# Optimization experiments

Measured on AMD Instinct MI355X. Metric: run time of the kernel, lower is better.

Reference implementation:

```python
import jax, jax.numpy as jnp
import numpy as np

R_MAX = 10.0
NUM_BESSEL = 8
POLY_P = 5
EMB = 64
MLP_DIM = 256
NUM_LAYERS = 3
IN_DIM = 10
OUT_DIM = 1
N_NODES = 256
N_EDGES = 1024
N_GRAPHS = 16
# gated TP output: 0e channel carries 64 scalars + 128 gates (one per gated 1o/2e irrep)
GATE_MUL = {0: 3 * EMB, 1: EMB, 2: EMB}
L0_PATHS = [(0, 0, 0), (0, 1, 1), (0, 2, 2)]  # in_irreps = 64x0e
LN_PATHS = [(0, 0, 0), (1, 1, 0), (2, 2, 0), (0, 1, 1), (1, 0, 1), (1, 2, 1), (2, 1, 1), (0, 2, 2), (2, 0, 2), (1, 1, 2), (2, 2, 2)]

def _npaths(paths):
    d = {0: 0, 1: 0, 2: 0}
    for _, _, l3 in paths:
        d[l3] += 1
    return d

L0_NP = _npaths(L0_PATHS)
LN_NP = _npaths(LN_PATHS)
L0_NUMEL = sum(EMB * GATE_MUL[l3] for _, _, l3 in L0_PATHS)   # 20480
LN_NUMEL = sum(EMB * GATE_MUL[l3] for _, _, l3 in LN_PATHS)   # 69632

# ---- real spherical harmonics, component normalization (||Y_l||^2 = 2l+1) ----
def _sh_np(v):
    x, y, z = v[:, 0], v[:, 1], v[:, 2]
    s15 = np.sqrt(15.0)
    return {0: np.ones((v.shape[0], 1)),
            1: np.sqrt(3.0) * np.stack([x, y, z], 1),
            2: np.stack([s15 * x * y, s15 * y * z, 0.5 * np.sqrt(5.0) * (3 * z * z - 1), s15 * x * z, 0.5 * s15 * (x * x - y * y)], 1)}

def _rot(axis, t):
    c, s = np.cos(t), np.sin(t)
    R = np.eye(3)
    i, j = [(1, 2), (2, 0), (0, 1)][axis]
    R[i, i] = c; R[j, j] = c; R[i, j] = -s; R[j, i] = s
    return R

_PTS = np.random.RandomState(0).randn(64, 3)
_PTS /= np.linalg.norm(_PTS, axis=1, keepdims=True)

def _D(l, R):
    # rep matrix D with Y(Rv) = D @ Y(v), fit by least squares over sample points
    A = _sh_np(_PTS)[l]
    B = _sh_np(_PTS @ R.T)[l]
    return np.linalg.lstsq(A, B, rcond=None)[0].T

def _gen(l, axis, eps=1e-4):
    return (_D(l, _rot(axis, eps)) - _D(l, _rot(axis, -eps))) / (2 * eps)

def _cg(l1, l2, l3):
    # Clebsch-Gordan tensor as null space of the infinitesimal equivariance constraint
    d1, d2, d3 = 2 * l1 + 1, 2 * l2 + 1, 2 * l3 + 1
    rows = []
    for a in range(3):
        J1, J2, J3 = _gen(l1, a), _gen(l2, a), _gen(l3, a)
        rows.append(np.kron(J1.T, np.eye(d2 * d3)) + np.kron(np.eye(d1), np.kron(J2.T, np.eye(d3))) - np.kron(np.eye(d1 * d2), J3))
    _, _, Vh = np.linalg.svd(np.vstack(rows))
    c = Vh[-1].reshape(d1, d2, d3)
    c = c / np.linalg.norm(c)
    c = c * np.sign(c.flat[int(np.argmax(np.abs(c)))])
    return c

CG = {p: jnp.asarray(_cg(*p), jnp.float32) for p in set(LN_PATHS)}

def _sh_jax(u):
    x, y, z = u[..., 0], u[..., 1], u[..., 2]
    s15 = 15.0 ** 0.5
    return {0: jnp.ones_like(x)[:, None],
            1: (3.0 ** 0.5) * jnp.stack([x, y, z], -1),
            2: jnp.stack([s15 * x * y, s15 * y * z, 0.5 * (5.0 ** 0.5) * (3 * z * z - 1), s15 * x * z, 0.5 * s15 * (x * x - y * y)], -1)}

def _radial(r):
    # Bessel radial basis * polynomial cutoff envelope (MACE-style RadialEmbeddingBlock)
    n = jnp.arange(1, NUM_BESSEL + 1, dtype=r.dtype)
    bessel = (2.0 / R_MAX) ** 0.5 * jnp.sin(n * jnp.pi * r[:, None] / R_MAX) / r[:, None]
    x = r / R_MAX
    p = POLY_P
    env = 1.0 - 0.5 * (p + 1) * (p + 2) * x ** p + p * (p + 2) * x ** (p + 1) - 0.5 * p * (p + 1) * x ** (p + 2)
    env = env * (x < 1.0)
    return bessel * env[:, None]

def _conv(h, sh, ef, recv, send, paths, n_per, w1, b1, w2, b2):
    # TensorProductConvLayer: MLP(edge_feats) -> TP weights, CG tensor product, scatter-sum, gate
    E = ef.shape[0]
    w = jax.nn.relu(ef @ w1 + b1) @ w2 + b2  # (E, weight_numel)
    msgs = {0: 0.0, 1: 0.0, 2: 0.0}
    off = 0
    for (l1, l2, l3) in paths:
        mv = GATE_MUL[l3]
        wp = w[:, off:off + EMB * mv].reshape(E, EMB, mv)
        off += EMB * mv
        tmp = jnp.einsum('eui,ej,ijk->euk', h[l1][send], sh[l2], CG[(l1, l2, l3)])
        alpha = float(1.0 / np.sqrt(EMB * n_per[l3]))  # fan-in path normalization
        msgs[l3] = msgs[l3] + alpha * jnp.einsum('euk,euv->evk', tmp, wp)
    agg = {l: jax.ops.segment_sum(msgs[l], recv, num_segments=N_NODES) for l in msgs}
    s = agg[0][..., 0]  # (N, 192): 64 scalars + 128 gates
    return {0: jax.nn.silu(s[:, :EMB])[:, :, None],
            1: agg[1] * jax.nn.sigmoid(s[:, EMB:2 * EMB])[:, :, None],
            2: agg[2] * jax.nn.sigmoid(s[:, 2 * EMB:])[:, :, None]}

def _forward(atoms, pos, edge_index, batch, emb, l0_fc1_w, l0_fc1_b, l0_fc2_w, l0_fc2_b, fcs1_w, fcs1_b, fcs2_w, fcs2_b, pred_w1, pred_b1, pred_w2, pred_b2):
    recv, send = edge_index[0], edge_index[1]
    vec = pos[recv] - pos[send]
    r = jnp.maximum(jnp.linalg.norm(vec, axis=-1), 1e-6)
    sh = _sh_jax(vec / r[:, None])
    ef = _radial(r)
    h = {0: emb[atoms][:, :, None]}  # (N, 64, 1) scalar features
    h_new = _conv(h, sh, ef, recv, send, L0_PATHS, L0_NP, l0_fc1_w, l0_fc1_b, l0_fc2_w, l0_fc2_b)
    h_new[0] = h_new[0] + h[0]  # residual; F.pad means only scalar block overlaps
    h = h_new
    for i in range(NUM_LAYERS - 1):
        h_new = _conv(h, sh, ef, recv, send, LN_PATHS, LN_NP, fcs1_w[i], fcs1_b[i], fcs2_w[i], fcs2_b[i])
        h = {l: h_new[l] + h[l] for l in h_new}
    pooled = jax.ops.segment_sum(h[0][..., 0], batch, num_segments=N_GRAPHS)  # out[:, :emb_dim]
    return jax.nn.relu(pooled @ pred_w1 + pred_b1) @ pred_w2 + pred_b2

def setup_inputs():
    key = jax.random.key(0)
    ks = jax.random.split(key, 12)
    def lin(k, fi, fo):
        return jax.random.normal(k, (fi, fo), jnp.float32) * float(1.0 / np.sqrt(fi))
    return dict(
        atoms=jax.random.randint(ks[0], (N_NODES,), 0, IN_DIM),
        pos=jax.random.normal(ks[1], (N_NODES, 3), jnp.float32) * 2.0,
        edge_index=jax.random.randint(ks[2], (2, N_EDGES), 0, N_NODES),
        batch=jnp.sort(jax.random.randint(ks[3], (N_NODES,), 0, N_GRAPHS)),
        emb=jax.random.normal(ks[4], (IN_DIM, EMB), jnp.float32),
        l0_fc1_w=lin(ks[5], NUM_BESSEL, MLP_DIM), l0_fc1_b=jnp.zeros((MLP_DIM,), jnp.float32),
        l0_fc2_w=lin(ks[6], MLP_DIM, L0_NUMEL), l0_fc2_b=jnp.zeros((L0_NUMEL,), jnp.float32),
        fcs1_w=jax.random.normal(ks[7], (NUM_LAYERS - 1, NUM_BESSEL, MLP_DIM), jnp.float32) * float(1.0 / np.sqrt(NUM_BESSEL)),
        fcs1_b=jnp.zeros((NUM_LAYERS - 1, MLP_DIM), jnp.float32),
        fcs2_w=jax.random.normal(ks[8], (NUM_LAYERS - 1, MLP_DIM, LN_NUMEL), jnp.float32) * float(1.0 / np.sqrt(MLP_DIM)),
        fcs2_b=jnp.zeros((NUM_LAYERS - 1, LN_NUMEL), jnp.float32),
        pred_w1=lin(ks[9], EMB, EMB), pred_b1=jnp.zeros((EMB,), jnp.float32),
        pred_w2=lin(ks[10], EMB, OUT_DIM), pred_b2=jnp.zeros((OUT_DIM,), jnp.float32),
    )

def reference(atoms, pos, edge_index, batch, emb, l0_fc1_w, l0_fc1_b, l0_fc2_w, l0_fc2_b, fcs1_w, fcs1_b, fcs2_w, fcs2_b, pred_w1, pred_b1, pred_w2, pred_b2):
    return _forward(atoms, pos, edge_index, batch, emb, l0_fc1_w, l0_fc1_b, l0_fc2_w, l0_fc2_b, fcs1_w, fcs1_b, fcs2_w, fcs2_b, pred_w1, pred_b1, pred_w2, pred_b2)
```

## Files before the change

### kernel.cpp

```cpp
#include <hip/hip_runtime.h>
#include <hip/hip_bf16.h>
#include <math.h>

#define NE 1024
#define NN 256
#define NG 16
#define EMB 64
#define KD 256
#define BK 64
#define NUMEL_L0 20480
#define NUMEL_LN 69632
#define MSGW 704
#define MAXE 256

typedef __attribute__((ext_vector_type(8))) __bf16 bf16x8;
typedef __attribute__((ext_vector_type(4))) float f32x4;
typedef __attribute__((ext_vector_type(4))) unsigned int u32x4;

__device__ __align__(16) float g_sh[NE * 8];
__device__ __align__(16) float g_ef[NE * 8];
__device__ __align__(16) unsigned short g_hidb[3][NE * KD];
__device__ __align__(16) unsigned short g_w2t0[(size_t)NUMEL_L0 * KD];
__device__ __align__(16) unsigned short g_w2t1[(size_t)NUMEL_LN * KD];
__device__ __align__(16) unsigned short g_w2t2[(size_t)NUMEL_LN * KD];
__device__ __align__(16) unsigned short g_wb0[(size_t)NE * NUMEL_L0];
__device__ __align__(16) unsigned short g_wb1[(size_t)NE * NUMEL_LN];
__device__ __align__(16) unsigned short g_wb2[(size_t)NE * NUMEL_LN];
__device__ __align__(16) float g_msgs[NE * MSGW];
__device__ __align__(16) float g_h0[NN * EMB];
__device__ __align__(16) float g_h1[NN * EMB * 3];
__device__ __align__(16) float g_h2[NN * EMB * 5];
__device__ int g_elist[NN * MAXE];
__device__ int g_ecnt[NN];
__device__ float g_cg[363];

__device__ __forceinline__ unsigned short f2b(float x) {
    __hip_bfloat16 h = __float2bfloat16(x);
    return *(unsigned short*)&h;
}
__device__ __forceinline__ float b2f(unsigned short u) {
    __hip_bfloat16 h;
    *(unsigned short*)&h = u;
    return __bfloat162float(h);
}

__device__ __forceinline__ void gld16(const void* g, void* l) {
    __builtin_amdgcn_global_load_lds(
        (const __attribute__((address_space(1))) unsigned int*)g,
        (__attribute__((address_space(3))) unsigned int*)l, 16, 0, 0);
}

struct Path { int l1, l2, d1, d2, d3, mv, off, cgoff, tmpoff; };

__constant__ Path PLN[11] = {
    {0, 0, 1, 1, 1, 192, 0,     0,   0},
    {1, 1, 3, 3, 1, 192, 12288, 1,   64},
    {2, 2, 5, 5, 1, 192, 24576, 10,  128},
    {0, 1, 1, 3, 3, 64,  36864, 35,  192},
    {1, 0, 3, 1, 3, 64,  40960, 44,  384},
    {1, 2, 3, 5, 3, 64,  45056, 53,  576},
    {2, 1, 5, 3, 3, 64,  49152, 98,  768},
    {0, 2, 1, 5, 5, 64,  53248, 143, 960},
    {2, 0, 5, 1, 5, 64,  57344, 168, 1280},
    {1, 1, 3, 3, 5, 64,  61440, 193, 1600},
    {2, 2, 5, 5, 5, 64,  65536, 238, 1920},
};
__constant__ Path PL0[3] = {
    {0, 0, 1, 1, 1, 192, 0,     0,   0},
    {0, 1, 1, 3, 3, 64,  12288, 35,  64},
    {0, 2, 1, 5, 5, 64,  16384, 143, 256},
};

__device__ void init_cg_body() {
    for (int i = 0; i < 363; i++) g_cg[i] = 0.f;
    const float K3 = 0.57735026918962576f;
    const float K5 = 0.44721359549995794f;
    const float A  = 0.31622776601683794f;
    const float B  = 0.18257418583505536f;
    const float C2 = 0.36514837167011072f;
    const float P  = 0.23904572186687872f;
    const float Q  = 0.20701966780270626f;
    const float S  = 0.11952286093343936f;
    g_cg[0] = 1.f;
    for (int i = 0; i < 3; i++) g_cg[1 + i * 3 + i] = K3;
    for (int i = 0; i < 5; i++) g_cg[10 + i * 5 + i] = K5;
    for (int i = 0; i < 3; i++) g_cg[35 + i * 3 + i] = K3;
    for (int i = 0; i < 3; i++) g_cg[44 + i * 3 + i] = K3;
    g_cg[53 + 1]  = A;  g_cg[53 + 15] = A;  g_cg[53 + 20] = A;
    g_cg[53 + 34] = A;  g_cg[53 + 11] = A;  g_cg[53 + 39] = A;
    g_cg[53 + 6]  = -B; g_cg[53 + 22] = -B; g_cg[53 + 38] = C2;
    g_cg[53 + 12] = A;  g_cg[53 + 28] = -A;
    g_cg[98 + 1]  = A;  g_cg[98 + 3]  = A;  g_cg[98 + 14] = A;
    g_cg[98 + 16] = A;  g_cg[98 + 29] = A;  g_cg[98 + 33] = A;
    g_cg[98 + 18] = -B; g_cg[98 + 22] = -B; g_cg[98 + 26] = C2;
    g_cg[98 + 36] = A;  g_cg[98 + 40] = -A;
    for (int i = 0; i < 5; i++) g_cg[143 + i * 5 + i] = K5;
    for (int i = 0; i < 5; i++) g_cg[168 + i * 5 + i] = K5;
    g_cg[193 + 5]  = A;  g_cg[193 + 15] = A;  g_cg[193 + 26] = A;
    g_cg[193 + 36] = A;  g_cg[193 + 13] = A;  g_cg[193 + 33] = A;
    g_cg[193 + 2]  = -B; g_cg[193 + 22] = -B; g_cg[193 + 42] = C2;
    g_cg[193 + 4]  = A;  g_cg[193 + 24] = -A;
    g_cg[238 + 2]   = P;  g_cg[238 + 10]  = P;  g_cg[238 + 50]  = P;
    g_cg[238 + 8]   = -Q; g_cg[238 + 16]  = -Q; g_cg[238 + 28]  = -Q;
    g_cg[238 + 40]  = -Q; g_cg[238 + 76]  = -Q; g_cg[238 + 80]  = -Q;
    g_cg[238 + 32]  = -S; g_cg[238 + 36]  = -S; g_cg[238 + 56]  = -S;
    g_cg[238 + 34]  = Q;  g_cg[238 + 46]  = Q;  g_cg[238 + 106] = Q;
    g_cg[238 + 62]  = -P;
    g_cg[238 + 74]  = P;  g_cg[238 + 114] = P;  g_cg[238 + 122] = P;
    g_cg[238 + 68]  = -S; g_cg[238 + 88]  = -S; g_cg[238 + 92]  = -S;
    g_cg[238 + 94]  = -Q; g_cg[238 + 98]  = -Q; g_cg[238 + 118] = -Q;
}

__global__ __launch_bounds__(256) void k_setup(const int* ei, const float* pos,
                                               const int* atoms, const float* emb) {
    int bid = blockIdx.x, tid = threadIdx.x;
    if (bid == 0) {
        if (tid == 0) init_cg_body();
        return;
    }
    if (bid <= 4) {
        int e = (bid - 1) * 256 + tid;
        int recv = ei[e], send = ei[NE + e];
        float vx = pos[recv * 3 + 0] - pos[send * 3 + 0];
        float vy = pos[recv * 3 + 1] - pos[send * 3 + 1];
        float vz = pos[recv * 3 + 2] - pos[send * 3 + 2];
        float rn = sqrtf(vx * vx + vy * vy + vz * vz);
        float r = fmaxf(rn, 1e-6f);
        float x = vx / r, y = vy / r, z = vz / r;
        const float S3 = 1.7320508075688772f;
        const float S15 = 3.8729833462074170f;
        const float S5H = 1.1180339887498949f;
        const float S15H = 1.9364916731037085f;
        g_sh[e * 8 + 0] = S3 * x;
        g_sh[e * 8 + 1] = S3 * y;
        g_sh[e * 8 + 2] = S3 * z;
        g_sh[e * 8 + 3] = S15 * x * y;
        g_sh[e * 8 + 4] = S15 * y * z;
        g_sh[e * 8 + 5] = S5H * (3.f * z * z - 1.f);
        g_sh[e * 8 + 6] = S15 * x * z;
        g_sh[e * 8 + 7] = S15H * (x * x - y * y);
        float xr = r * 0.1f;
        float env = 0.f;
        if (xr < 1.f) {
            float x5 = xr * xr * xr * xr * xr;
            env = 1.f - 21.f * x5 + 35.f * x5 * xr - 15.f * x5 * xr * xr;
        }
        const float SB = 0.44721359549995794f;
        const float PI = 3.14159265358979323846f;
        for (int nb = 1; nb <= 8; nb++) {
            g_ef[e * 8 + nb - 1] = SB * sinf((float)nb * PI * r * 0.1f) / r * env;
        }
        return;
    }
    if (bid <= 68) {
        int idx = (bid - 5) * 256 + tid;
        int n = idx / EMB, u = idx % EMB;
        g_h0[idx] = emb[atoms[n] * EMB + u];
        for (int k = 0; k < 3; k++) g_h1[idx * 3 + k] = 0.f;
        for (int k = 0; k < 5; k++) g_h2[idx * 5 + k] = 0.f;
        return;
    }
    {
        int n = bid - 69;
        int lane = tid & 63, w = tid >> 6;
        __shared__ int wsum[4];
        int mask = 0;
#pragma unroll
        for (int i = 0; i < 4; i++) {
            if (ei[tid * 4 + i] == n) mask |= 1 << i;
        }
        int nm = __popc(mask);
        int incl = nm;
#pragma unroll
        for (int off = 1; off < 64; off <<= 1) {
            int v = __shfl_up(incl, off);
            if (lane >= off) incl += v;
        }
        if (lane == 63) wsum[w] = incl;
        __syncthreads();
        int wbase = 0;
        for (int i = 0; i < w; i++) wbase += wsum[i];
        int base = wbase + incl - nm;
#pragma unroll
        for (int i = 0; i < 4; i++) {
            if (mask & (1 << i)) g_elist[n * MAXE + base++] = tid * 4 + i;
        }
        if (tid == 255) g_ecnt[n] = wbase + incl;
    }
}

__global__ __launch_bounds__(256) void k_w2t_hid_all(
        const float* l0w2, const float* f2w,
        const float* l0w1, const float* l0b1, const float* f1w, const float* f1b) {
    __shared__ float t[32][33];
    int bid = blockIdx.x;
    if (bid < 39936) {
        int layer, lbid, numel;
        const float* w2;
        unsigned short* dst;
        if (bid < 5120)       { layer = 0; lbid = bid;          numel = NUMEL_L0; w2 = l0w2; dst = g_w2t0; }
        else if (bid < 22528) { layer = 1; lbid = bid - 5120;   numel = NUMEL_LN; w2 = f2w;  dst = g_w2t1; }
        else                  { layer = 2; lbid = bid - 22528;  numel = NUMEL_LN;
                                w2 = f2w + (size_t)KD * NUMEL_LN; dst = g_w2t2; }
        int n0 = (lbid >> 3) * 32, k0 = (lbid & 7) * 32;
        int tx = threadIdx.x & 31, ty = threadIdx.x >> 5;
#pragma unroll
        for (int i = 0; i < 4; i++) {
            int kl = ty * 4 + i;
            t[kl][tx] = w2[(size_t)(k0 + kl) * numel + n0 + tx];
        }
        __syncthreads();
#pragma unroll
        for (int i = 0; i < 4; i++) {
            int nl = ty * 4 + i;
            dst[(size_t)(n0 + nl) * KD + k0 + tx] = f2b(t[tx][nl]);
        }
    } else {
        int r = bid - 39936;
        int layer = r >> 10, e = r & 1023;
        const float* w1 = layer == 0 ? l0w1 : f1w + (size_t)(layer - 1) * 8 * KD;
        const float* b1 = layer == 0 ? l0b1 : f1b + (size_t)(layer - 1) * KD;
        int m = threadIdx.x;
        float acc = b1[m];
        for (int nb = 0; nb < 8; nb++) acc += g_ef[e * 8 + nb] * w1[nb * KD + m];
        g_hidb[layer][e * KD + m] = f2b(fmaxf(acc, 0.f));
    }
}

__global__ __launch_bounds__(256) void k_gemm_all(const float* l0b2, const float* f2b_) {
    __shared__ unsigned short S[16384];
    int tid = threadIdx.x;
    int lane = tid & 63, wid = tid >> 6;
    int wm = wid >> 1, wn = wid & 1;
    int id = blockIdx.x;
    int layer, lid, numel;
    const unsigned short* hidb;
    const unsigned short* w2t;
    unsigned short* wb;
    const float* b2;
    if (id < 4352)      { layer = 2; lid = id;        numel = NUMEL_LN; hidb = g_hidb[2]; w2t = g_w2t2; wb = g_wb2; b2 = f2b_ + NUMEL_LN; }
    else if (id < 8704) { layer = 1; lid = id - 4352; numel = NUMEL_LN; hidb = g_hidb[1]; w2t = g_w2t1; wb = g_wb1; b2 = f2b_; }
    else                { layer = 0; lid = id - 8704; numel = NUMEL_L0; hidb = g_hidb[0]; w2t = g_w2t0; wb = g_wb0; b2 = l0b2; }
    int xcd = lid & 7;
    int q = lid >> 3;
    int mb = q & 7;
    int ytile = q >> 3;
    int nt = xcd + 8 * ytile;
    int m0 = mb * 128, n0 = nt * 128;
    int fr = lane & 15;
    int ko = (lane >> 4) * 8;

    const char* gA = (const char*)hidb;
    const char* gB = (const char*)w2t;
    f32x4 acc[4][4] = {};

    for (int kst = 0; kst < 4; kst++) {
#pragma unroll
        for (int i = 0; i < 4; i++) {
            int L = wid * 4096 + i * 1024 + lane * 16;
            int row = L >> 7, p = L & 127;
            int sp = p ^ ((row & 7) << 4);
            gld16(gA + ((size_t)(m0 + row) * KD + kst * BK) * 2 + sp, (char*)S + L);
        }
#pragma unroll
        for (int i = 0; i < 4; i++) {
            int L = wid * 4096 + i * 1024 + lane * 16;
            int row = L >> 7, p = L & 127;
            int sp = p ^ ((row & 7) << 4);
            gld16(gB + ((size_t)(n0 + row) * KD + kst * BK) * 2 + sp, (char*)S + 16384 + L);
        }
        __syncthreads();
#pragma unroll
        for (int ks = 0; ks < 2; ks++) {
            int klb = ks * 64 + ko * 2;
            bf16x8 af[4], bf_[4];
#pragma unroll
            for (int f = 0; f < 4; f++) {
                int ra = wm * 64 + f * 16 + fr;
                af[f] = *(bf16x8*)((char*)S + ra * 128 + (klb ^ ((ra & 7) << 4)));
                int rb = wn * 64 + f * 16 + fr;
                bf_[f] = *(bf16x8*)((char*)S + 16384 + rb * 128 + (klb ^ ((rb & 7) << 4)));
            }
#pragma unroll
            for (int i = 0; i < 4; i++)
#pragma unroll
                for (int j = 0; j < 4; j++)
                    acc[i][j] = __builtin_amdgcn_mfma_f32_16x16x32_bf16(af[i], bf_[j], acc[i][j], 0, 0, 0);
        }
        __syncthreads();
    }

#pragma unroll
    for (int j = 0; j < 4; j++) {
        int colL = wn * 64 + j * 16 + fr;
        float bb = b2[n0 + colL];
#pragma unroll
        for (int i = 0; i < 4; i++) {
#pragma unroll
            for (int r = 0; r < 4; r++) {
                int rowL = wm * 64 + i * 16 + (lane >> 4) * 4 + r;
                *(unsigned short*)((char*)S + rowL * 256 + ((colL * 2) ^ ((rowL & 7) << 4))) =
                    f2b(acc[i][j][r] + bb);
            }
        }
    }
    __syncthreads();
    for (int c = tid; c < 2048; c += 256) {
        int row = c >> 4, p16 = (c & 15) * 16;
        u32x4 v = *(u32x4*)((char*)S + row * 256 + (p16 ^ ((row & 7) << 4)));
        *(u32x4*)((char*)(wb + (size_t)(m0 + row) * numel + n0) + p16) = v;
    }
}

__global__ __launch_bounds__(256) void k_contract(const int* ei, int layer) {
    int e = blockIdx.x;
    int grp = blockIdx.y;
    int tid = threadIdx.x;
    __shared__ float tmp[1280];
    int layer0 = (layer == 0) ? 1 : 0;
    int numel = layer0 ? NUMEL_L0 : NUMEL_LN;
    const unsigned short* wbase = layer == 0 ? g_wb0 : (layer == 1 ? g_wb1 : g_wb2);
    const Path* PT = layer0 ? PL0 : PLN;
    int npaths = layer0 ? 3 : 11;
    int pstart = layer0 ? grp : (grp == 0 ? 0 : (grp == 1 ? 3 : 7));
    int pend   = layer0 ? grp + 1 : (grp == 0 ? 3 : (grp == 1 ? 7 : 11));
    int tbase = PT[pstart].tmpoff;
    int tend  = (pend < npaths) ? PT[pend].tmpoff : (layer0 ? 576 : 2240);
    int ttot = tend - tbase;
    const unsigned short* wrow = wbase + (size_t)e * numel;
    int send = ei[NE + e];

    for (int t = tid; t < ttot; t += 256) {
        int tt = t + tbase;
        int p = pend - 1;
        while (tt < PT[p].tmpoff) p--;
        Path pp = PT[p];
        int rem = tt - pp.tmpoff;
        int u = rem / pp.d3, k = rem % pp.d3;
        float acc = 0.f;
        for (int i = 0; i < pp.d1; i++) {
            float hv = (pp.l1 == 0) ? g_h0[send * EMB + u]
                     : (pp.l1 == 1) ? g_h1[(send * EMB + u) * 3 + i]
                                    : g_h2[(send * EMB + u) * 5 + i];
            for (int j = 0; j < pp.d2; j++) {
                float sv = (pp.l2 == 0) ? 1.f
                         : (pp.l2 == 1 ? g_sh[e * 8 + j] : g_sh[e * 8 + 3 + j]);
                acc += hv * sv * g_cg[pp.cgoff + (i * pp.d2 + j) * pp.d3 + k];
            }
        }
        tmp[t] = acc;
    }
    __syncthreads();

    float alpha0 = layer0 ? 0.125f : 0.07216878364870323f;
    float alpha12 = layer0 ? 0.125f : 0.0625f;
    int v3 = tid / 3, k3 = tid - v3 * 3;
    int v5a = tid / 5, k5a = tid - v5a * 5;
    int p5b = 256 + tid;
    int v5b = p5b / 5, k5b = p5b - v5b * 5;
    float a0 = 0.f, a1 = 0.f;

    for (int p = pstart; p < pend; p++) {
        Path pp = PT[p];
        int to = pp.tmpoff - tbase;
        const unsigned short* wp = wrow + pp.off;
        if (pp.d3 == 1) {
            if (tid < 192) {
#pragma unroll 16
                for (int u = 0; u < 64; u++)
                    a0 += tmp[to + u] * b2f(wp[u * 192 + tid]);
            }
        } else if (pp.d3 == 3) {
            if (tid < 192) {
#pragma unroll 16
                for (int u = 0; u < 64; u++)
                    a0 += tmp[to + u * 3 + k3] * b2f(wp[u * 64 + v3]);
            }
        } else {
#pragma unroll 16
            for (int u = 0; u < 64; u++)
                a0 += tmp[to + u * 5 + k5a] * b2f(wp[u * 64 + v5a]);
            if (tid < 64) {
#pragma unroll 16
                for (int u = 0; u < 64; u++)
                    a1 += tmp[to + u * 5 + k5b] * b2f(wp[u * 64 + v5b]);
            }
        }
    }
    if (grp == 0) {
        if (tid < 192) g_msgs[e * MSGW + tid] = alpha0 * a0;
    } else if (grp == 1) {
        if (tid < 192) g_msgs[e * MSGW + 192 + tid] = alpha12 * a0;
    } else {
        g_msgs[e * MSGW + 384 + tid] = alpha12 * a0;
        if (tid < 64) g_msgs[e * MSGW + 640 + tid] = alpha12 * a1;
    }
}

__global__ __launch_bounds__(256) void k_agggate() {
    int n = blockIdx.x, tid = threadIdx.x;
    __shared__ float agg[MSGW];
    int cnt = g_ecnt[n];
    for (int d = tid; d < MSGW; d += 256) {
        float a = 0.f;
        for (int idx = 0; idx < cnt; idx++) {
            int e = g_elist[n * MAXE + idx];
            a += g_msgs[e * MSGW + d];
        }
        agg[d] = a;
    }
    __syncthreads();
    if (tid < EMB) {
        int u = tid;
        float s0 = agg[u], s1 = agg[64 + u], s2 = agg[128 + u];
        float sg0 = 1.f / (1.f + expf(-s0));
        float g0 = s0 * sg0;
        float sg1 = 1.f / (1.f + expf(-s1));
        float sg2 = 1.f / (1.f + expf(-s2));
        g_h0[n * EMB + u] += g0;
        for (int k = 0; k < 3; k++) g_h1[(n * EMB + u) * 3 + k] += agg[192 + u * 3 + k] * sg1;
        for (int k = 0; k < 5; k++) g_h2[(n * EMB + u) * 5 + k] += agg[384 + u * 5 + k] * sg2;
    }
}

__global__ __launch_bounds__(1024) void k_poolhead(const int* batch, const float* w1,
                                                   const float* b1, const float* w2,
                                                   const float* b2, float* out) {
    __shared__ float pl[NG * EMB];
    int g = threadIdx.x >> 6, u = threadIdx.x & 63;
    float a = 0.f;
    for (int n = 0; n < NN; n++)
        if (batch[n] == g) a += g_h0[n * EMB + u];
    pl[g * EMB + u] = a;
    __syncthreads();
    float t = b1[u];
    for (int uu = 0; uu < EMB; uu++) t += pl[g * EMB + uu] * w1[uu * EMB + u];
    t = fmaxf(t, 0.f);
    float contrib = t * w2[u];
    for (int off = 32; off > 0; off >>= 1) contrib += __shfl_down(contrib, off);
    if (u == 0) out[g] = contrib + b2[0];
}

extern "C" void kernel_launch(void* const* d_in, const int* in_sizes, int n_in,
                              void* d_out, int out_size, void* d_ws, size_t ws_size,
                              hipStream_t stream) {
    const int* atoms = (const int*)d_in[0];
    const float* pos = (const float*)d_in[1];
    const int* ei = (const int*)d_in[2];
    const int* batch = (const int*)d_in[3];
    const float* emb = (const float*)d_in[4];
    const float* l0w1 = (const float*)d_in[5];
    const float* l0b1 = (const float*)d_in[6];
    const float* l0w2 = (const float*)d_in[7];
    const float* l0b2 = (const float*)d_in[8];
    const float* f1w = (const float*)d_in[9];
    const float* f1b = (const float*)d_in[10];
    const float* f2w = (const float*)d_in[11];
    const float* f2b_ = (const float*)d_in[12];
    const float* pw1 = (const float*)d_in[13];
    const float* pb1 = (const float*)d_in[14];
    const float* pw2 = (const float*)d_in[15];
    const float* pb2 = (const float*)d_in[16];
    float* out = (float*)d_out;

    k_setup<<<dim3(325), dim3(256), 0, stream>>>(ei, pos, atoms, emb);
    k_w2t_hid_all<<<dim3(43008), dim3(256), 0, stream>>>(l0w2, f2w, l0w1, l0b1, f1w, f1b);
    k_gemm_all<<<dim3(9984), dim3(256), 0, stream>>>(l0b2, f2b_);

    for (int layer = 0; layer < 3; layer++) {
        k_contract<<<dim3(NE, 3), dim3(256), 0, stream>>>(ei, layer);
        k_agggate<<<dim3(NN), dim3(256), 0, stream>>>();
    }

    k_poolhead<<<dim3(1), dim3(1024), 0, stream>>>(batch, pw1, pb1, pw2, pb2, out);
}
```

Before: 474.5 us.

## Run per-layer weight GEMM just before contraction with a shared output buffer

Replaces the single batched GEMM that produced all three layers' per-edge weight tensors with one GEMM launch per layer, issued right before that layer's contraction. All three layers now write into one shared bf16 buffer, so a freshly written weight tensor is likely still in cache when the contraction reads it, and the global footprint shrinks. The weight transpose is merged into the setup kernel and the hidden-layer MLP gets its own kernel. In exchange there are more launches, and the per-layer GEMMs are serialized with the contraction and aggregation kernels instead of running as one large grid.

```diff
diff --git a/kernel.cpp b/kernel.cpp
--- a/kernel.cpp
+++ b/kernel.cpp
@@ -23,9 +23,7 @@
 __device__ __align__(16) unsigned short g_w2t0[(size_t)NUMEL_L0 * KD];
 __device__ __align__(16) unsigned short g_w2t1[(size_t)NUMEL_LN * KD];
 __device__ __align__(16) unsigned short g_w2t2[(size_t)NUMEL_LN * KD];
-__device__ __align__(16) unsigned short g_wb0[(size_t)NE * NUMEL_L0];
-__device__ __align__(16) unsigned short g_wb1[(size_t)NE * NUMEL_LN];
-__device__ __align__(16) unsigned short g_wb2[(size_t)NE * NUMEL_LN];
+__device__ __align__(16) unsigned short g_wb[(size_t)NE * NUMEL_LN];
 __device__ __align__(16) float g_msgs[NE * MSGW];
 __device__ __align__(16) float g_h0[NN * EMB];
 __device__ __align__(16) float g_h1[NN * EMB * 3];
@@ -112,7 +110,8 @@
 }
 
 __global__ __launch_bounds__(256) void k_setup(const int* ei, const float* pos,
-                                               const int* atoms, const float* emb) {
+                                               const int* atoms, const float* emb,
+                                               const float* l0w2, const float* f2w) {
     int bid = blockIdx.x, tid = threadIdx.x;
     if (bid == 0) {
         if (tid == 0) init_cg_body();
@@ -160,7 +159,7 @@
         for (int k = 0; k < 5; k++) g_h2[idx * 5 + k] = 0.f;
         return;
     }
-    {
+    if (bid <= 324) {
         int n = bid - 69;
         int lane = tid & 63, w = tid >> 6;
         __shared__ int wsum[4];
@@ -186,24 +185,20 @@
             if (mask & (1 << i)) g_elist[n * MAXE + base++] = tid * 4 + i;
         }
         if (tid == 255) g_ecnt[n] = wbase + incl;
-    }
-}
-
-__global__ __launch_bounds__(256) void k_w2t_hid_all(
-        const float* l0w2, const float* f2w,
-        const float* l0w1, const float* l0b1, const float* f1w, const float* f1b) {
-    __shared__ float t[32][33];
-    int bid = blockIdx.x;
-    if (bid < 39936) {
-        int layer, lbid, numel;
+        return;
+    }
+    {
+        __shared__ float t[32][33];
+        int wbid = bid - 325;
+        int lbid, numel;
         const float* w2;
         unsigned short* dst;
-        if (bid < 5120)       { layer = 0; lbid = bid;          numel = NUMEL_L0; w2 = l0w2; dst = g_w2t0; }
-        else if (bid < 22528) { layer = 1; lbid = bid - 5120;   numel = NUMEL_LN; w2 = f2w;  dst = g_w2t1; }
-        else                  { layer = 2; lbid = bid - 22528;  numel = NUMEL_LN;
-                                w2 = f2w + (size_t)KD * NUMEL_LN; dst = g_w2t2; }
+        if (wbid < 5120)       { lbid = wbid;         numel = NUMEL_L0; w2 = l0w2; dst = g_w2t0; }
+        else if (wbid < 22528) { lbid = wbid - 5120;  numel = NUMEL_LN; w2 = f2w;  dst = g_w2t1; }
+        else                   { lbid = wbid - 22528; numel = NUMEL_LN;
+                                 w2 = f2w + (size_t)KD * NUMEL_LN; dst = g_w2t2; }
         int n0 = (lbid >> 3) * 32, k0 = (lbid & 7) * 32;
-        int tx = threadIdx.x & 31, ty = threadIdx.x >> 5;
+        int tx = tid & 31, ty = tid >> 5;
 #pragma unroll
         for (int i = 0; i < 4; i++) {
             int kl = ty * 4 + i;
@@ -215,34 +210,29 @@
             int nl = ty * 4 + i;
             dst[(size_t)(n0 + nl) * KD + k0 + tx] = f2b(t[tx][nl]);
         }
-    } else {
-        int r = bid - 39936;
-        int layer = r >> 10, e = r & 1023;
-        const float* w1 = layer == 0 ? l0w1 : f1w + (size_t)(layer - 1) * 8 * KD;
-        const float* b1 = layer == 0 ? l0b1 : f1b + (size_t)(layer - 1) * KD;
-        int m = threadIdx.x;
-        float acc = b1[m];
-        for (int nb = 0; nb < 8; nb++) acc += g_ef[e * 8 + nb] * w1[nb * KD + m];
-        g_hidb[layer][e * KD + m] = f2b(fmaxf(acc, 0.f));
-    }
-}
-
-__global__ __launch_bounds__(256) void k_gemm_all(const float* l0b2, const float* f2b_) {
+    }
+}
+
+__global__ __launch_bounds__(256) void k_hid_all(const float* l0w1, const float* l0b1,
+                                                 const float* f1w, const float* f1b) {
+    int r = blockIdx.x;
+    int layer = r >> 10, e = r & 1023;
+    const float* w1 = layer == 0 ? l0w1 : f1w + (size_t)(layer - 1) * 8 * KD;
+    const float* b1 = layer == 0 ? l0b1 : f1b + (size_t)(layer - 1) * KD;
+    int m = threadIdx.x;
+    float acc = b1[m];
+    for (int nb = 0; nb < 8; nb++) acc += g_ef[e * 8 + nb] * w1[nb * KD + m];
+    g_hidb[layer][e * KD + m] = f2b(fmaxf(acc, 0.f));
+}
+
+__global__ __launch_bounds__(256) void k_gemm_mfma(const float* b2, int numel, int layer) {
     __shared__ unsigned short S[16384];
     int tid = threadIdx.x;
     int lane = tid & 63, wid = tid >> 6;
     int wm = wid >> 1, wn = wid & 1;
     int id = blockIdx.x;
-    int layer, lid, numel;
-    const unsigned short* hidb;
-    const unsigned short* w2t;
-    unsigned short* wb;
-    const float* b2;
-    if (id < 4352)      { layer = 2; lid = id;        numel = NUMEL_LN; hidb = g_hidb[2]; w2t = g_w2t2; wb = g_wb2; b2 = f2b_ + NUMEL_LN; }
-    else if (id < 8704) { layer = 1; lid = id - 4352; numel = NUMEL_LN; hidb = g_hidb[1]; w2t = g_w2t1; wb = g_wb1; b2 = f2b_; }
-    else                { layer = 0; lid = id - 8704; numel = NUMEL_L0; hidb = g_hidb[0]; w2t = g_w2t0; wb = g_wb0; b2 = l0b2; }
-    int xcd = lid & 7;
-    int q = lid >> 3;
+    int xcd = id & 7;
+    int q = id >> 3;
     int mb = q & 7;
     int ytile = q >> 3;
     int nt = xcd + 8 * ytile;
@@ -250,7 +240,8 @@
     int fr = lane & 15;
     int ko = (lane >> 4) * 8;
 
-    const char* gA = (const char*)hidb;
+    const unsigned short* w2t = layer == 0 ? g_w2t0 : (layer == 1 ? g_w2t1 : g_w2t2);
+    const char* gA = (const char*)g_hidb[layer];
     const char* gB = (const char*)w2t;
     f32x4 acc[4][4] = {};
 
@@ -308,7 +299,7 @@
     for (int c = tid; c < 2048; c += 256) {
         int row = c >> 4, p16 = (c & 15) * 16;
         u32x4 v = *(u32x4*)((char*)S + row * 256 + (p16 ^ ((row & 7) << 4)));
-        *(u32x4*)((char*)(wb + (size_t)(m0 + row) * numel + n0) + p16) = v;
+        *(u32x4*)((char*)(g_wb + (size_t)(m0 + row) * numel + n0) + p16) = v;
     }
 }
 
@@ -319,7 +310,6 @@
     __shared__ float tmp[1280];
     int layer0 = (layer == 0) ? 1 : 0;
     int numel = layer0 ? NUMEL_L0 : NUMEL_LN;
-    const unsigned short* wbase = layer == 0 ? g_wb0 : (layer == 1 ? g_wb1 : g_wb2);
     const Path* PT = layer0 ? PL0 : PLN;
     int npaths = layer0 ? 3 : 11;
     int pstart = layer0 ? grp : (grp == 0 ? 0 : (grp == 1 ? 3 : 7));
@@ -327,7 +317,7 @@
     int tbase = PT[pstart].tmpoff;
     int tend  = (pend < npaths) ? PT[pend].tmpoff : (layer0 ? 576 : 2240);
     int ttot = tend - tbase;
-    const unsigned short* wrow = wbase + (size_t)e * numel;
+    const unsigned short* wrow = g_wb + (size_t)e * numel;
     int send = ei[NE + e];
 
     for (int t = tid; t < ttot; t += 256) {
@@ -463,11 +453,13 @@
     const float* pb2 = (const float*)d_in[16];
     float* out = (float*)d_out;
 
-    k_setup<<<dim3(325), dim3(256), 0, stream>>>(ei, pos, atoms, emb);
-    k_w2t_hid_all<<<dim3(43008), dim3(256), 0, stream>>>(l0w2, f2w, l0w1, l0b1, f1w, f1b);
-    k_gemm_all<<<dim3(9984), dim3(256), 0, stream>>>(l0b2, f2b_);
+    k_setup<<<dim3(40261), dim3(256), 0, stream>>>(ei, pos, atoms, emb, l0w2, f2w);
+    k_hid_all<<<dim3(3072), dim3(256), 0, stream>>>(l0w1, l0b1, f1w, f1b);
 
     for (int layer = 0; layer < 3; layer++) {
+        const float* b2 = layer == 0 ? l0b2 : f2b_ + (size_t)(layer - 1) * NUMEL_LN;
+        int numel = layer == 0 ? NUMEL_L0 : NUMEL_LN;
+        k_gemm_mfma<<<dim3((numel / 128) * (NE / 128)), dim3(256), 0, stream>>>(b2, numel, layer);
         k_contract<<<dim3(NE, 3), dim3(256), 0, stream>>>(ei, layer);
         k_agggate<<<dim3(NN), dim3(256), 0, stream>>>();
     }
```

After: 421.3 us (median of 3 runs). 11.2% less time.
